# Performance work log

Hardware: AMD Instinct MI355X
Metric: run time of the kernel (lower is better)

## Reference

```python
import jax, jax.numpy as jnp
import numpy as np

# dims
B, S, E, H = 2, 2048, 2048, 2688   # batch, seq, embedding_dim, hidden_dim
NH, DH = 4, 2688 // 4              # mLSTM heads, head dim
KS = 4                             # causal conv kernel size
BLK = 4                            # qkv_proj_blocksize
NPH = H // BLK                     # headwise-proj heads


def setup_inputs() -> dict:
    key = jax.random.key(0)
    ks = jax.random.split(key, 12)
    r = lambda i, shape, s=0.02: jax.random.normal(ks[i], shape, jnp.float32) * s
    return dict(
        x=jax.random.normal(ks[0], (B, S, E), jnp.float32),
        W_in=r(1, (E, 2 * H)),                       # up projection (no bias)
        conv_w=r(2, (KS, 1, H), 0.1),                # depthwise causal conv kernel (W, I/g, O)
        conv_b=jnp.zeros((H,), jnp.float32),
        Wq=r(3, (NPH, BLK, BLK), 0.3),               # headwise q proj
        Wk=r(4, (NPH, BLK, BLK), 0.3),               # headwise k proj
        Wv=r(5, (NPH, BLK, BLK), 0.3),               # headwise v proj
        W_ig=r(6, (3 * H, NH)),                      # input gate proj
        b_ig=jax.random.normal(ks[7], (NH,), jnp.float32),
        W_fg=r(8, (3 * H, NH)),                      # forget gate proj
        b_fg=jnp.linspace(3.0, 6.0, NH).astype(jnp.float32),
        norm_w=jnp.ones((H,), jnp.float32),          # multi-head layernorm weight
        skip=jnp.ones((H,), jnp.float32),            # learnable skip
        W_out=r(9, (H, E)),                          # down projection
    )


def _headwise(x, W):
    # LinearHeadwiseExpand: (B,S,H) -> (B,S,NPH,BLK) -> einsum -> (B,S,H)
    b, s, _ = x.shape
    xh = x.reshape(b, s, NPH, BLK)
    return jnp.einsum('bshd,hdo->bsho', xh, W).reshape(b, s, -1)


def reference(x, W_in, conv_w, conv_b, Wq, Wk, Wv, W_ig, b_ig, W_fg, b_fg, norm_w, skip, W_out):
    x_inner = x @ W_in                               # (B,S,2H)
    x_m, z = jnp.split(x_inner, 2, axis=-1)
    # depthwise causal conv1d
    xc = jax.lax.conv_general_dilated(
        x_m, conv_w, (1,), [(KS - 1, 0)],
        dimension_numbers=('NWC', 'WIO', 'NWC'), feature_group_count=H) + conv_b
    xca = jax.nn.silu(xc)
    q = _headwise(xca, Wq)
    k = _headwise(xca, Wk)
    v = _headwise(x_m, Wv)
    # ---- mLSTM cell (parallel stabilized form) ----
    qh = q.reshape(B, S, NH, DH).transpose(0, 2, 1, 3)   # (B,NH,S,DH)
    kh = k.reshape(B, S, NH, DH).transpose(0, 2, 1, 3)
    vh = v.reshape(B, S, NH, DH).transpose(0, 2, 1, 3)
    if_in = jnp.concatenate([q, k, v], axis=-1)          # (B,S,3H)
    i_pre = (if_in @ W_ig + b_ig).transpose(0, 2, 1)     # (B,NH,S)
    f_pre = (if_in @ W_fg + b_fg).transpose(0, 2, 1)
    log_fg = jax.nn.log_sigmoid(f_pre)                   # (B,NH,S)
    cs = jnp.cumsum(log_fg, axis=-1)
    # log decay matrix: sum of log forget gates t=j+1..i, causal masked
    dmat = cs[:, :, :, None] - cs[:, :, None, :]         # (B,NH,S,S)
    mask = jnp.tril(jnp.ones((S, S), bool))
    log_D = jnp.where(mask, dmat + i_pre[:, :, None, :], -jnp.inf)
    m = jnp.max(log_D, axis=-1, keepdims=True)           # stabilizer (B,NH,S,1)
    D = jnp.exp(log_D - m)
    qk = jnp.einsum('bnsd,bntd->bnst', qh, kh) / jnp.sqrt(jnp.float32(DH))
    C = qk * D
    n = jnp.maximum(jnp.abs(C.sum(-1, keepdims=True)), jnp.exp(-m))
    h = jnp.einsum('bnst,bntd->bnsd', C / (n + 1e-6), vh)
    # multi-head layernorm over DH, learnable scale over full H
    mu = h.mean(-1, keepdims=True)
    var = h.var(-1, keepdims=True)
    hn = (h - mu) * jax.lax.rsqrt(var + 1e-5)
    hn = hn.transpose(0, 2, 1, 3).reshape(B, S, H) * norm_w
    # ---- gated skip + output ----
    h_skip = hn + skip * xca
    hs = h_skip * jax.nn.silu(z)
    return hs @ W_out
```

## Files before the change

kernel.cpp:

```cpp
#include <hip/hip_runtime.h>

typedef unsigned short u16;
typedef unsigned int u32;
typedef __bf16 bf16x8 __attribute__((ext_vector_type(8)));
typedef float f32x4 __attribute__((ext_vector_type(4)));

#define BB   2
#define SS   2048
#define EE   2048
#define HH   2688
#define NHH  4
#define DHH  672
#define NPHH 672
#define H2   5376
#define H3   8064

__device__ __forceinline__ float b2f(u16 u) {
  union { unsigned int i; float f; } c; c.i = ((unsigned int)u) << 16; return c.f;
}
__device__ __forceinline__ u16 f2b(float f) {
  union { float f; unsigned int i; } c; c.f = f;
  unsigned int i = c.i;
  return (u16)((i + 0x7FFFu + ((i >> 16) & 1u)) >> 16);
}
__device__ __forceinline__ float silu_f(float x) { return x / (1.f + __expf(-x)); }
__device__ __forceinline__ float logsig_f(float f) {
  return (f >= 0.f) ? -log1pf(__expf(-f)) : (f - log1pf(__expf(f)));
}

__device__ __forceinline__ void gl2lds16(const u16* g, u16* s) {
  __builtin_amdgcn_global_load_lds(
      (const __attribute__((address_space(1))) u32*)g,
      (__attribute__((address_space(3))) u32*)s, 16, 0, 0);
}

template <int N> __device__ __forceinline__ void vmwait() {
  asm volatile("s_waitcnt vmcnt(%0)" :: "n"(N) : "memory");
}

template <int MODE, int OUTF32>
__global__ __launch_bounds__(512, 1) void gemm8(
    const u16* __restrict__ A, const u16* __restrict__ Bt, void* __restrict__ Cp,
    int M, int N, int K, int lda, int ldb, int ldc,
    long sAhi, long sAlo, long sBhi, long sBlo, long sChi, long sClo,
    const float* __restrict__ aux1, const float* __restrict__ aux2,
    int auxStride, int causal)
{
  constexpr int SLOT = (128 + 256) * 64;
  __shared__ __align__(16) u16 sm[3 * SLOT];

  int gx = gridDim.x;
  int nwg = gx * gridDim.y;
  int flat = blockIdx.y * gx + blockIdx.x;
  int qq = nwg >> 3, r8 = nwg & 7;
  int xcd = flat & 7, seq = flat >> 3;
  int logical = (xcd < r8 ? xcd * (qq + 1) : r8 * (qq + 1) + (xcd - r8) * qq) + seq;
  int bx = logical % gx, by = logical / gx;
  int m0 = by * 128, n0 = bx * 256;
  if (MODE == 1 && n0 > m0 + 127) return;

  int bz = blockIdx.z, bzh = bz >> 2, bzl = bz & 3;
  A  += bzh * sAhi + bzl * sAlo;
  Bt += bzh * sBhi + bzl * sBlo;
  const float* a1 = aux1 ? aux1 + (long)bz * auxStride : nullptr;
  const float* a2 = aux2 ? aux2 + (long)bz * auxStride : nullptr;
  u16*   C16 = (u16*)Cp + bzh * sChi + bzl * sClo;
  float* C32 = (float*)Cp + bzh * sChi + bzl * sClo;

  int t = threadIdx.x, lane = t & 63, w = t >> 6;
  int l15 = lane & 15, quad = lane >> 4;
  int wr = w >> 2, wc = w & 3;

  int srow = t >> 3;
  int sw8 = ((t & 7) ^ (srow & 7)) * 8;
  const u16* pS[6];
  int dOf[6];
#pragma unroll
  for (int c = 0; c < 2; ++c) {
    pS[c] = A + (long)(m0 + c * 64 + srow) * lda + sw8;
    dOf[c] = c * 4096 + w * 512;
  }
#pragma unroll
  for (int c = 0; c < 4; ++c) {
    pS[2 + c] = Bt + (long)(n0 + c * 64 + srow) * ldb + sw8;
    dOf[2 + c] = 8192 + c * 4096 + w * 512;
  }

  f32x4 acc[4][4];
#pragma unroll
  for (int i = 0; i < 4; i++)
#pragma unroll
    for (int j = 0; j < 4; j++) acc[i][j] = (f32x4){0.f, 0.f, 0.f, 0.f};

  int Keff = (MODE == 2 && causal) ? min(K, m0 + 128) : K;
  int T = Keff >> 6;

  auto STAGE = [&](int slot, int k2, int c) {
    gl2lds16(pS[c] + k2, sm + slot * SLOT + dOf[c]);
  };

  int npre = T < 2 ? T : 2;
  for (int tt = 0; tt < npre; ++tt)
#pragma unroll
    for (int c = 0; c < 6; ++c) STAGE(tt, tt << 6, c);
  if (npre >= 2) vmwait<6>(); else vmwait<0>();
  __builtin_amdgcn_s_barrier();
  __builtin_amdgcn_sched_barrier(0);

  int sl = 0;
  for (int tq = 0; tq < T; ++tq) {
    u16* Sb = sm + sl * SLOT;
    int sl2 = sl + 2; if (sl2 >= 3) sl2 -= 3;
    const bool stg = (tq + 2 < T);
    const int k2 = (tq + 2) << 6;
    int cx = (l15 & 7);

    bf16x8 bfr[4][2], af[2][2];
#pragma unroll
    for (int j = 0; j < 4; ++j)
#pragma unroll
      for (int ks = 0; ks < 2; ++ks)
        bfr[j][ks] = *reinterpret_cast<const bf16x8*>(
            Sb + 8192 + (wc * 64 + j * 16 + l15) * 64 + ((((ks << 2) + quad) ^ cx) << 3));
#pragma unroll
    for (int i = 0; i < 2; ++i)
#pragma unroll
      for (int ks = 0; ks < 2; ++ks)
        af[i][ks] = *reinterpret_cast<const bf16x8*>(
            Sb + (wr * 64 + i * 16 + l15) * 64 + ((((ks << 2) + quad) ^ cx) << 3));
    if (stg) { STAGE(sl2, k2, 0); STAGE(sl2, k2, 1); STAGE(sl2, k2, 2); }
    __builtin_amdgcn_s_barrier();
    asm volatile("s_waitcnt lgkmcnt(0)" ::: "memory");
    __builtin_amdgcn_sched_barrier(0);
    __builtin_amdgcn_s_setprio(1);
#pragma unroll
    for (int i = 0; i < 2; ++i)
#pragma unroll
      for (int j = 0; j < 4; ++j) {
        acc[i][j] = __builtin_amdgcn_mfma_f32_16x16x32_bf16(af[i][0], bfr[j][0], acc[i][j], 0, 0, 0);
        acc[i][j] = __builtin_amdgcn_mfma_f32_16x16x32_bf16(af[i][1], bfr[j][1], acc[i][j], 0, 0, 0);
      }
    __builtin_amdgcn_s_setprio(0);
    __builtin_amdgcn_sched_barrier(0);
    __builtin_amdgcn_s_barrier();

    bf16x8 ag[2][2];
#pragma unroll
    for (int i = 0; i < 2; ++i)
#pragma unroll
      for (int ks = 0; ks < 2; ++ks)
        ag[i][ks] = *reinterpret_cast<const bf16x8*>(
            Sb + (wr * 64 + (i + 2) * 16 + l15) * 64 + ((((ks << 2) + quad) ^ cx) << 3));
    if (stg) { STAGE(sl2, k2, 3); STAGE(sl2, k2, 4); STAGE(sl2, k2, 5); }
    __builtin_amdgcn_s_barrier();
    asm volatile("s_waitcnt lgkmcnt(0)" ::: "memory");
    __builtin_amdgcn_sched_barrier(0);
    __builtin_amdgcn_s_setprio(1);
#pragma unroll
    for (int i = 0; i < 2; ++i)
#pragma unroll
      for (int j = 0; j < 4; ++j) {
        acc[i + 2][j] = __builtin_amdgcn_mfma_f32_16x16x32_bf16(ag[i][0], bfr[j][0], acc[i + 2][j], 0, 0, 0);
        acc[i + 2][j] = __builtin_amdgcn_mfma_f32_16x16x32_bf16(ag[i][1], bfr[j][1], acc[i + 2][j], 0, 0, 0);
      }
    __builtin_amdgcn_s_setprio(0);
    __builtin_amdgcn_sched_barrier(0);
    if (tq + 1 < T) {
      if (stg) vmwait<6>(); else vmwait<0>();
      __builtin_amdgcn_s_barrier();
      __builtin_amdgcn_sched_barrier(0);
    }
    sl = sl + 1; if (sl >= 3) sl = 0;
  }

  const float rs = 0.03857583749f;
#pragma unroll
  for (int i = 0; i < 4; i++) {
#pragma unroll
    for (int j = 0; j < 4; j++) {
      int col = n0 + wc * 64 + j * 16 + l15;
      if (col >= N) continue;
#pragma unroll
      for (int rr = 0; rr < 4; rr++) {
        int row = m0 + wr * 64 + i * 16 + quad * 4 + rr;
        if (row >= M) continue;
        float v = acc[i][j][rr];
        if (MODE == 1) v = (col <= row) ? v * rs * __expf(a1[col] - a2[row]) : 0.f;
        else if (MODE == 2) v = v * a1[row];
        if (OUTF32) C32[(long)row * ldc + col] = v;
        else        C16[(long)row * ldc + col] = f2b(v);
      }
    }
  }
}

template <int BM, int MODE, int OUTF32>
__global__ __launch_bounds__(512, 1) void gemm_p(
    const u16* __restrict__ A, const u16* __restrict__ Bt, void* __restrict__ Cp,
    int M, int N, int K, int lda, int ldb, int ldc,
    long sAhi, long sAlo, long sBhi, long sBlo, long sChi, long sClo,
    const float* __restrict__ aux1, const float* __restrict__ aux2,
    int auxStride, int causal)
{
  constexpr int MFR   = BM / 32;
  constexpr int NPH   = MFR / 2;
  constexpr int SLOT  = (BM + 256) * 32;
  constexpr int ACH   = BM / 128;
  constexpr int LOADS = ACH + 2;
  __shared__ __align__(16) u16 sm[4 * SLOT];

  int gx = gridDim.x;
  int nwg = gx * gridDim.y;
  int flat = blockIdx.y * gx + blockIdx.x;
  int qq = nwg >> 3, r8 = nwg & 7;
  int xcd = flat & 7, seq = flat >> 3;
  int logical = (xcd < r8 ? xcd * (qq + 1) : r8 * (qq + 1) + (xcd - r8) * qq) + seq;
  int bx = logical % gx, by = logical / gx;
  int m0 = by * BM, n0 = bx * 256;
  if (MODE == 1 && n0 > m0 + BM - 1) return;

  int bz = blockIdx.z, bzh = bz >> 2, bzl = bz & 3;
  A  += bzh * sAhi + bzl * sAlo;
  Bt += bzh * sBhi + bzl * sBlo;
  const float* a1 = aux1 ? aux1 + (long)bz * auxStride : nullptr;
  const float* a2 = aux2 ? aux2 + (long)bz * auxStride : nullptr;
  u16*   C16 = (u16*)Cp + bzh * sChi + bzl * sClo;
  float* C32 = (float*)Cp + bzh * sChi + bzl * sClo;

  int t = threadIdx.x, lane = t & 63, w = t >> 6;
  int l15 = lane & 15, quad = lane >> 4;
  int wr = w >> 2, wc = w & 3;

  int srow = t >> 2;
  int swz = (((t & 3) ^ ((t >> 3) & 3)) * 8);
  const u16* pS[LOADS];
  int coff[LOADS];
#pragma unroll
  for (int c = 0; c < ACH; ++c) {
    pS[c] = A + (long)(m0 + c * 128 + srow) * lda + swz;
    coff[c] = c * 4096 + w * 512;
  }
#pragma unroll
  for (int c = 0; c < 2; ++c) {
    pS[ACH + c] = Bt + (long)(n0 + c * 128 + srow) * ldb + swz;
    coff[ACH + c] = BM * 32 + c * 4096 + w * 512;
  }

  int rswz = (quad ^ ((l15 >> 1) & 3)) * 8;
  int aoff = (wr * (BM / 2) + l15) * 32 + rswz;
  int boff = BM * 32 + (wc * 64 + l15) * 32 + rswz;

  f32x4 acc[MFR][4];
#pragma unroll
  for (int i = 0; i < MFR; i++)
#pragma unroll
    for (int j = 0; j < 4; j++) acc[i][j] = (f32x4){0.f, 0.f, 0.f, 0.f};

  int Keff = (MODE == 2 && causal) ? min(K, m0 + BM) : K;
  int T = Keff >> 5;

  auto STAGE1 = [&](int tt, int c) {
    gl2lds16(pS[c] + (tt << 5), sm + (tt & 3) * SLOT + coff[c]);
  };

  int npre = T < 3 ? T : 3;
  for (int tt = 0; tt < npre; ++tt)
#pragma unroll
    for (int c = 0; c < LOADS; ++c) STAGE1(tt, c);
  if (npre >= 3)      vmwait<2 * LOADS>();
  else if (npre == 2) vmwait<LOADS>();
  else                vmwait<0>();
  __builtin_amdgcn_s_barrier();
  __builtin_amdgcn_sched_barrier(0);

  for (int tq = 0; tq < T; ++tq) {
    u16* Sb = sm + (tq & 3) * SLOT;
    const bool stg = (tq + 3 < T);
    bf16x8 bf[4];
#pragma unroll
    for (int p = 0; p < NPH; ++p) {
      bf16x8 a0 = *reinterpret_cast<const bf16x8*>(Sb + aoff + (2 * p) * 512);
      bf16x8 a1v = *reinterpret_cast<const bf16x8*>(Sb + aoff + (2 * p + 1) * 512);
      if (p == 0) {
#pragma unroll
        for (int j = 0; j < 4; ++j)
          bf[j] = *reinterpret_cast<const bf16x8*>(Sb + boff + j * 512);
      }
      if (stg) {
#pragma unroll
        for (int c = p * LOADS / NPH; c < (p + 1) * LOADS / NPH; ++c)
          STAGE1(tq + 3, c);
      }
      __builtin_amdgcn_s_barrier();
      asm volatile("s_waitcnt lgkmcnt(0)" ::: "memory");
      __builtin_amdgcn_sched_barrier(0);
      __builtin_amdgcn_s_setprio(1);
#pragma unroll
      for (int j = 0; j < 4; ++j)
        acc[2 * p][j] = __builtin_amdgcn_mfma_f32_16x16x32_bf16(a0, bf[j], acc[2 * p][j], 0, 0, 0);
#pragma unroll
      for (int j = 0; j < 4; ++j)
        acc[2 * p + 1][j] = __builtin_amdgcn_mfma_f32_16x16x32_bf16(a1v, bf[j], acc[2 * p + 1][j], 0, 0, 0);
      __builtin_amdgcn_s_setprio(0);
      __builtin_amdgcn_sched_barrier(0);
    }
    if (tq + 1 < T) {
      if (tq + 3 < T)      vmwait<2 * LOADS>();
      else if (tq + 2 < T) vmwait<LOADS>();
      else                 vmwait<0>();
      __builtin_amdgcn_s_barrier();
      __builtin_amdgcn_sched_barrier(0);
    }
  }

  const float rs = 0.03857583749f;
#pragma unroll
  for (int i = 0; i < MFR; i++) {
#pragma unroll
    for (int j = 0; j < 4; j++) {
      int col = n0 + wc * 64 + j * 16 + l15;
      if (col >= N) continue;
#pragma unroll
      for (int rr = 0; rr < 4; rr++) {
        int row = m0 + wr * (BM / 2) + i * 16 + quad * 4 + rr;
        if (row >= M) continue;
        float v = acc[i][j][rr];
        if (MODE == 1) v = (col <= row) ? v * rs * __expf(a1[col] - a2[row]) : 0.f;
        else if (MODE == 2) v = v * a1[row];
        if (OUTF32) C32[(long)row * ldc + col] = v;
        else        C16[(long)row * ldc + col] = f2b(v);
      }
    }
  }
}

template <int F32IN>
__global__ __launch_bounds__(256) void transpose_any(
    const void* __restrict__ in, u16* __restrict__ out, int R, int C, int ldin,
    long inHi, long inLo, long outStride)
{
  __shared__ u16 tile[64][65];
  int bz = blockIdx.z, bzh = bz >> 2, bzl = bz & 3;
  const u16* in16 = (const u16*)in + bzh * inHi + bzl * inLo;
  const float* inf = (const float*)in + bzh * inHi + bzl * inLo;
  out += (long)bz * outStride;
  int r0 = blockIdx.y * 64, c0 = blockIdx.x * 64;
  int t = threadIdx.x;
  for (int idx = t; idx < 64 * 64; idx += 256) {
    int r = idx >> 6, c = idx & 63;
    int rr = r0 + r, cc = c0 + c;
    u16 v = 0;
    if (rr < R && cc < C) {
      long off = (long)rr * ldin + cc;
      v = F32IN ? f2b(inf[off]) : in16[off];
    }
    tile[r][c] = v;
  }
  __syncthreads();
  for (int idx = t; idx < 64 * 64; idx += 256) {
    int r = idx & 63, c = idx >> 6;
    int rr = r0 + r, cc = c0 + c;
    if (rr < R && cc < C) out[(long)cc * R + rr] = tile[r][c];
  }
}

__global__ __launch_bounds__(256) void convert_x(
    const float* __restrict__ x, u16* __restrict__ o)
{
  long i = ((long)blockIdx.x * 256 + threadIdx.x) * 8;
  if (i >= (long)4096 * EE) return;
  float4 a = *reinterpret_cast<const float4*>(x + i);
  float4 b = *reinterpret_cast<const float4*>(x + i + 4);
  u16 t8[8] = {f2b(a.x), f2b(a.y), f2b(a.z), f2b(a.w),
               f2b(b.x), f2b(b.y), f2b(b.z), f2b(b.w)};
  *reinterpret_cast<uint4*>(o + i) = *reinterpret_cast<uint4*>(t8);
}

__global__ __launch_bounds__(256) void prep_wqkv(
    const float* __restrict__ Wq, const float* __restrict__ Wk,
    const float* __restrict__ Wv, u16* __restrict__ o)
{
  int i = blockIdx.x * 256 + threadIdx.x;
  if (i >= 3 * 10752) return;
  int m = i / 10752, j = i % 10752;
  const float* W = (m == 0) ? Wq : (m == 1) ? Wk : Wv;
  o[i] = f2b(W[j]);
}

__global__ __launch_bounds__(256) void conv_head(
    const u16* __restrict__ xinner, const float* __restrict__ cw,
    const float* __restrict__ cb, const u16* __restrict__ Wqkv,
    u16* __restrict__ xca, u16* __restrict__ q, u16* __restrict__ k,
    u16* __restrict__ v)
{
  long idx = (long)blockIdx.x * 256 + threadIdx.x;
  if (idx >= (long)BB * SS * NPHH) return;
  int nph = (int)(idx % NPHH);
  long bs = idx / NPHH;
  int s = (int)(bs % SS);
  int h4 = nph * 4;
  float4 acc = *reinterpret_cast<const float4*>(cb + h4);
  uint2 xmr;
#pragma unroll
  for (int w = 0; w < 4; w++) {
    int sp = s + w - 3;
    if (sp < 0) continue;
    uint2 xr = *reinterpret_cast<const uint2*>(xinner + (bs + w - 3) * H2 + h4);
    if (w == 3) xmr = xr;
    const u16* xh = (const u16*)&xr;
    float4 cwv = *reinterpret_cast<const float4*>(cw + w * HH + h4);
    acc.x += b2f(xh[0]) * cwv.x;
    acc.y += b2f(xh[1]) * cwv.y;
    acc.z += b2f(xh[2]) * cwv.z;
    acc.w += b2f(xh[3]) * cwv.w;
  }
  float xaf[4] = {silu_f(acc.x), silu_f(acc.y), silu_f(acc.z), silu_f(acc.w)};
  u16 xa16[4] = {f2b(xaf[0]), f2b(xaf[1]), f2b(xaf[2]), f2b(xaf[3])};
#pragma unroll
  for (int d = 0; d < 4; d++) xaf[d] = b2f(xa16[d]);
  const u16* xm = (const u16*)&xmr;
  float xmf[4];
#pragma unroll
  for (int d = 0; d < 4; d++) xmf[d] = b2f(xm[d]);
  *reinterpret_cast<uint2*>(xca + bs * HH + h4) = *reinterpret_cast<uint2*>(xa16);

  union { uint4 v4[2]; u16 h[16]; } wq, wk, wv;
  const uint4* wqp = reinterpret_cast<const uint4*>(Wqkv + nph * 16);
  const uint4* wkp = reinterpret_cast<const uint4*>(Wqkv + 10752 + nph * 16);
  const uint4* wvp = reinterpret_cast<const uint4*>(Wqkv + 21504 + nph * 16);
  wq.v4[0] = wqp[0]; wq.v4[1] = wqp[1];
  wk.v4[0] = wkp[0]; wk.v4[1] = wkp[1];
  wv.v4[0] = wvp[0]; wv.v4[1] = wvp[1];
  u16 qo[4], ko[4], vo[4];
#pragma unroll
  for (int o = 0; o < 4; o++) {
    float aq = 0.f, ak = 0.f, av = 0.f;
#pragma unroll
    for (int d = 0; d < 4; d++) {
      aq += xaf[d] * b2f(wq.h[d * 4 + o]);
      ak += xaf[d] * b2f(wk.h[d * 4 + o]);
      av += xmf[d] * b2f(wv.h[d * 4 + o]);
    }
    qo[o] = f2b(aq); ko[o] = f2b(ak); vo[o] = f2b(av);
  }
  long ob = bs * HH + h4;
  *reinterpret_cast<uint2*>(q + ob) = *reinterpret_cast<uint2*>(qo);
  *reinterpret_cast<uint2*>(k + ob) = *reinterpret_cast<uint2*>(ko);
  *reinterpret_cast<uint2*>(v + ob) = *reinterpret_cast<uint2*>(vo);
}

__global__ __launch_bounds__(256) void gate_gemv(
    const u16* __restrict__ qb, const u16* __restrict__ kb,
    const u16* __restrict__ vb, const float* __restrict__ Wig,
    const float* __restrict__ Wfg, float* __restrict__ G)
{
  __shared__ u16 wlds[8 * HH];
  int seg = blockIdx.y;
  const u16* X = (seg == 0) ? qb : (seg == 1) ? kb : vb;
  int t = threadIdx.x;
  for (int c = t; c < HH; c += 256) {
    float4 wi = *reinterpret_cast<const float4*>(Wig + ((long)seg * HH + c) * 4);
    float4 wf = *reinterpret_cast<const float4*>(Wfg + ((long)seg * HH + c) * 4);
    wlds[0 * HH + c] = f2b(wi.x); wlds[1 * HH + c] = f2b(wi.y);
    wlds[2 * HH + c] = f2b(wi.z); wlds[3 * HH + c] = f2b(wi.w);
    wlds[4 * HH + c] = f2b(wf.x); wlds[5 * HH + c] = f2b(wf.y);
    wlds[6 * HH + c] = f2b(wf.z); wlds[7 * HH + c] = f2b(wf.w);
  }
  __syncthreads();
  int wv = t >> 6, lane = t & 63;
  int r0 = blockIdx.x * 32 + wv * 8;
  for (int r = 0; r < 8; ++r) {
    int row = r0 + r;
    const u16* xr = X + (long)row * HH;
    float a0=0,a1=0,a2=0,a3=0,a4=0,a5=0,a6=0,a7=0;
    for (int ch = lane; ch < HH / 8; ch += 64) {
      uint4 xv = *reinterpret_cast<const uint4*>(xr + ch * 8);
      const u16* xe = (const u16*)&xv;
      float xf[8];
#pragma unroll
      for (int e = 0; e < 8; ++e) xf[e] = b2f(xe[e]);
#pragma unroll
      for (int j = 0; j < 8; ++j) {
        uint4 wv4 = *reinterpret_cast<const uint4*>(wlds + j * HH + ch * 8);
        const u16* we = (const u16*)&wv4;
        float s = 0.f;
#pragma unroll
        for (int e = 0; e < 8; ++e) s += xf[e] * b2f(we[e]);
        if (j == 0) a0 += s; else if (j == 1) a1 += s;
        else if (j == 2) a2 += s; else if (j == 3) a3 += s;
        else if (j == 4) a4 += s; else if (j == 5) a5 += s;
        else if (j == 6) a6 += s; else a7 += s;
      }
    }
#pragma unroll
    for (int off = 32; off > 0; off >>= 1) {
      a0 += __shfl_down(a0, off); a1 += __shfl_down(a1, off);
      a2 += __shfl_down(a2, off); a3 += __shfl_down(a3, off);
      a4 += __shfl_down(a4, off); a5 += __shfl_down(a5, off);
      a6 += __shfl_down(a6, off); a7 += __shfl_down(a7, off);
    }
    if (lane == 0) {
      float* g = G + ((long)seg * 4096 + row) * 24 + seg * 8;
      g[0] = a0; g[1] = a1; g[2] = a2; g[3] = a3;
      g[4] = a4; g[5] = a5; g[6] = a6; g[7] = a7;
    }
  }
}

__global__ __launch_bounds__(1024) void scan_kernel(
    const float* __restrict__ G, const float* __restrict__ big,
    const float* __restrict__ bfg,
    float* __restrict__ avec, float* __restrict__ rmaxvec, float* __restrict__ mvec)
{
  __shared__ float buf[2][SS];
  __shared__ float isave[SS];
  __shared__ float cssave[SS];
  int bn = blockIdx.x;
  int b = bn >> 2, n = bn & 3;
  int t = threadIdx.x;
  float bi = big[n], bf = bfg[n];
  for (int i = t; i < SS; i += 1024) {
    long tk = (long)b * SS + i;
    float ip = G[tk * 24 + n] + G[(4096 + tk) * 24 + 8 + n] +
               G[(8192 + tk) * 24 + 16 + n] + bi;
    float fp = G[tk * 24 + 4 + n] + G[(4096 + tk) * 24 + 12 + n] +
               G[(8192 + tk) * 24 + 20 + n] + bf;
    isave[i] = ip;
    buf[0][i] = logsig_f(fp);
  }
  __syncthreads();
  int src = 0;
  for (int off = 1; off < SS; off <<= 1) {
    int dst = 1 - src;
    for (int i = t; i < SS; i += 1024) {
      float x = buf[src][i];
      if (i >= off) x += buf[src][i - off];
      buf[dst][i] = x;
    }
    __syncthreads();
    src = dst;
  }
  for (int i = t; i < SS; i += 1024) {
    float cs = buf[src][i];
    cssave[i] = cs;
    float a = isave[i] - cs;
    avec[(long)bn * SS + i] = a;
    buf[src][i] = a;
  }
  __syncthreads();
  for (int off = 1; off < SS; off <<= 1) {
    int dst = 1 - src;
    for (int i = t; i < SS; i += 1024) {
      float x = buf[src][i];
      if (i >= off) x = fmaxf(x, buf[src][i - off]);
      buf[dst][i] = x;
    }
    __syncthreads();
    src = dst;
  }
  for (int i = t; i < SS; i += 1024) {
    rmaxvec[(long)bn * SS + i] = buf[src][i];
    mvec[(long)bn * SS + i] = cssave[i] + buf[src][i];
  }
}

__global__ __launch_bounds__(256) void rowsum_kernel(
    const u16* __restrict__ P, const float* __restrict__ mvec, float* __restrict__ invn,
    long Pstride)
{
  int bz = blockIdx.z;
  P += (long)bz * Pstride;
  mvec += (long)bz * SS;
  invn += (long)bz * SS;
  int row = (blockIdx.x * 256 + threadIdx.x) >> 6;
  int lane = threadIdx.x & 63;
  if (row >= SS) return;
  const u16* pr = P + (long)row * SS;
  float s = 0.f;
  int j0 = lane * 8;
  for (; j0 + 7 <= row; j0 += 512) {
    uint4 u = *reinterpret_cast<const uint4*>(pr + j0);
    const u16* e = (const u16*)&u;
#pragma unroll
    for (int q = 0; q < 8; ++q) s += b2f(e[q]);
  }
  if (j0 <= row) {
    for (int q = 0; j0 + q <= row; ++q) s += b2f(pr[j0 + q]);
  }
#pragma unroll
  for (int off = 32; off > 0; off >>= 1) s += __shfl_down(s, off);
  if (lane == 0) {
    float n = fmaxf(fabsf(s), __expf(-mvec[row]));
    invn[row] = 1.f / (n + 1e-6f);
  }
}

__global__ __launch_bounds__(256) void ln_skip_gate(
    const u16* __restrict__ h, const u16* __restrict__ xca,
    const u16* __restrict__ xinner, const float* __restrict__ normw,
    const float* __restrict__ skipw, u16* __restrict__ hs)
{
  int row = (blockIdx.x * 256 + threadIdx.x) >> 6;
  int lane = threadIdx.x & 63;
  if (row >= BB * NHH * SS) return;
  int s = row % SS;
  int n = (row / SS) % NHH;
  int b = row / (SS * NHH);
  const u16* hr = h + (long)row * DHH;
  float sum = 0.f, ss = 0.f;
  float vx[6], vy[6];
#pragma unroll
  for (int i = 0; i < 6; ++i) {
    int d2 = lane + i * 64;
    float x = 0.f, y = 0.f;
    if (d2 < DHH / 2) {
      u32 u = *reinterpret_cast<const u32*>(hr + d2 * 2);
      x = b2f((u16)u); y = b2f((u16)(u >> 16));
    }
    vx[i] = x; vy[i] = y;
    sum += x + y; ss += x * x + y * y;
  }
#pragma unroll
  for (int off = 32; off > 0; off >>= 1) { sum += __shfl_down(sum, off); ss += __shfl_down(ss, off); }
  sum = __shfl(sum, 0); ss = __shfl(ss, 0);
  float mu = sum / (float)DHH;
  float var = ss / (float)DHH - mu * mu;
  float rstd = rsqrtf(var + 1e-5f);
  long bs = (long)b * SS + s;
#pragma unroll
  for (int i = 0; i < 6; ++i) {
    int d2 = lane + i * 64;
    if (d2 >= DHH / 2) continue;
    int c = n * DHH + d2 * 2;
    float2 nw = *reinterpret_cast<const float2*>(normw + c);
    float2 sw = *reinterpret_cast<const float2*>(skipw + c);
    u32 xcu = *reinterpret_cast<const u32*>(xca + bs * HH + c);
    u32 zu  = *reinterpret_cast<const u32*>(xinner + bs * H2 + HH + c);
    float h0 = (vx[i] - mu) * rstd * nw.x + sw.x * b2f((u16)xcu);
    float h1 = (vy[i] - mu) * rstd * nw.y + sw.y * b2f((u16)(xcu >> 16));
    float o0 = h0 * silu_f(b2f((u16)zu));
    float o1 = h1 * silu_f(b2f((u16)(zu >> 16)));
    u32 ou = (u32)f2b(o0) | ((u32)f2b(o1) << 16);
    *reinterpret_cast<u32*>(hs + bs * HH + c) = ou;
  }
}

__global__ __launch_bounds__(256) void fill_sentinel(float* out, float v, long n) {
  long i = (long)blockIdx.x * 256 + threadIdx.x;
  if (i < n) out[i] = v;
}

extern "C" void kernel_launch(void* const* d_in, const int* in_sizes, int n_in,
                              void* d_out, int out_size, void* d_ws, size_t ws_size,
                              hipStream_t stream)
{
  const float* x      = (const float*)d_in[0];
  const float* W_in   = (const float*)d_in[1];
  const float* conv_w = (const float*)d_in[2];
  const float* conv_b = (const float*)d_in[3];
  const float* Wq     = (const float*)d_in[4];
  const float* Wk     = (const float*)d_in[5];
  const float* Wv     = (const float*)d_in[6];
  const float* W_ig   = (const float*)d_in[7];
  const float* b_ig   = (const float*)d_in[8];
  const float* W_fg   = (const float*)d_in[9];
  const float* b_fg   = (const float*)d_in[10];
  const float* norm_w = (const float*)d_in[11];
  const float* skipw  = (const float*)d_in[12];
  const float* W_out  = (const float*)d_in[13];
  float* out = (float*)d_out;
  const long SD = (long)SS * DHH;
  const long SP = (long)SS * SS;
  const long BH = (long)SS * HH;

  u16* ws = (u16*)d_ws;
  size_t off = 0;
  auto alloc = [&](size_t n) { u16* p = ws + off; off += n; return p; };
  u16* x_inner = alloc((size_t)4096 * H2);
  u16* xca     = alloc((size_t)4096 * HH);
  u16* qb      = alloc((size_t)4096 * HH);
  u16* kb      = alloc((size_t)4096 * HH);
  u16* vb      = alloc((size_t)4096 * HH);
  float* fvec  = (float*)(ws + off);
  off += 4 * 16384 * 2;
  float* avec    = fvec;
  float* rmaxvec = avec + 16384;
  float* mvec    = rmaxvec + 16384;
  float* invn    = mvec + 16384;
  u16* vt8 = alloc((size_t)8 * SD);
  u16* Pb8 = alloc((size_t)8 * SP);
  size_t need = off * 2;
  long outn = (long)4096 * EE;

  if (ws_size < need) {
    fill_sentinel<<<dim3((outn + 255) / 256), 256, 0, stream>>>(
        out, 200.f + 0.01f * (float)(ws_size >> 20), outn);
    return;
  }

  u16* W_inT  = qb;
  u16* xbf    = kb;
  u16* W_outT = vb;
  u16* hbuf   = kb;
  u16* hsbuf  = qb;
  float* G    = (float*)(Pb8 + 344064);
  u16* Wqkv   = Pb8 + 933888;

  prep_wqkv<<<dim3(126, 1, 1), 256, 0, stream>>>(Wq, Wk, Wv, Wqkv);
  transpose_any<1><<<dim3(84, 32, 1), 256, 0, stream>>>(
      W_in, W_inT, EE, H2, H2, 0, 0, 0);
  convert_x<<<dim3(4096, 1, 1), 256, 0, stream>>>(x, xbf);
  gemm8<0, 0><<<dim3(21, 32, 1), 512, 0, stream>>>(
      xbf, W_inT, x_inner, 4096, H2, EE, EE, EE, H2,
      0, 0, 0, 0, 0, 0, nullptr, nullptr, 0, 0);
  conv_head<<<dim3(10752, 1, 1), 256, 0, stream>>>(
      x_inner, conv_w, conv_b, Wqkv, xca, qb, kb, vb);
  gate_gemv<<<dim3(128, 3, 1), 256, 0, stream>>>(qb, kb, vb, W_ig, W_fg, G);
  scan_kernel<<<dim3(8, 1, 1), 1024, 0, stream>>>(G, b_ig, b_fg, avec, rmaxvec, mvec);
  transpose_any<0><<<dim3(11, 32, 8), 256, 0, stream>>>(
      vb, vt8, SS, DHH, HH, BH, DHH, SD);
  gemm_p<256, 1, 0><<<dim3(8, 8, 8), 512, 0, stream>>>(
      qb, kb, Pb8, SS, SS, DHH, HH, HH, SS,
      BH, DHH, BH, DHH, 4 * SP, SP, avec, rmaxvec, SS, 0);
  rowsum_kernel<<<dim3(512, 1, 8), 256, 0, stream>>>(Pb8, mvec, invn, SP);
  gemm8<2, 0><<<dim3(3, 16, 8), 512, 0, stream>>>(
      Pb8, vt8, hbuf, SS, DHH, SS, SS, SS, DHH,
      4 * SP, SP, 4 * SD, SD, 4 * SD, SD, invn, nullptr, SS, 1);
  transpose_any<1><<<dim3(32, 42, 1), 256, 0, stream>>>(
      W_out, W_outT, HH, EE, EE, 0, 0, 0);
  ln_skip_gate<<<dim3(4096, 1, 1), 256, 0, stream>>>(
      hbuf, xca, x_inner, norm_w, skipw, hsbuf);
  gemm8<0, 1><<<dim3(8, 32, 1), 512, 0, stream>>>(
      hsbuf, W_outT, out, 4096, EE, HH, HH, HH, EE,
      0, 0, 0, 0, 0, 0, nullptr, nullptr, 0, 0);
}
```

Measured before the change: 651.5 us.

## Fuse gate projections into conv_head and replace scan with warp-shuffle scan

The input/forget gate GEMV moves into conv_head. Each block now handles one (batch, seq) row, so the fp32 q/k/v values multiply pre-packed bf16 gate weights and are reduced in-block, with no re-read of q/k/v from global memory. The separate gate_gemv kernel goes away and a small weight-prep kernel is added. The scan kernel changes from a log-step shared-memory Hillis-Steele scan with many barriers to a per-thread serial plus warp-shuffle scan. Gate preactivations now use unrounded fp32 q/k/v, which slightly changes numerics versus before.

```diff
diff --git a/kernel.cpp b/kernel.cpp
--- a/kernel.cpp
+++ b/kernel.cpp
@@ -387,180 +387,182 @@
   o[i] = f2b(W[j]);
 }
 
-__global__ __launch_bounds__(256) void conv_head(
+__global__ __launch_bounds__(256) void prep_gatew(
+    const float* __restrict__ Wig, const float* __restrict__ Wfg,
+    u16* __restrict__ Wg)
+{
+  int i = blockIdx.x * 256 + threadIdx.x;
+  if (i >= NPHH * 96) return;
+  int nph = i / 96, r = i % 96;
+  int seg = r >> 5, d = (r >> 3) & 3, j = r & 7;
+  const float* W = (j < 4) ? Wig : Wfg;
+  Wg[i] = f2b(W[(long)(seg * HH + nph * 4 + d) * 4 + (j & 3)]);
+}
+
+__global__ __launch_bounds__(704) void conv_head(
     const u16* __restrict__ xinner, const float* __restrict__ cw,
     const float* __restrict__ cb, const u16* __restrict__ Wqkv,
-    u16* __restrict__ xca, u16* __restrict__ q, u16* __restrict__ k,
-    u16* __restrict__ v)
-{
-  long idx = (long)blockIdx.x * 256 + threadIdx.x;
-  if (idx >= (long)BB * SS * NPHH) return;
-  int nph = (int)(idx % NPHH);
-  long bs = idx / NPHH;
+    const u16* __restrict__ Wg, u16* __restrict__ xca, u16* __restrict__ q,
+    u16* __restrict__ k, u16* __restrict__ v, float* __restrict__ G2)
+{
+  __shared__ float gsh[8];
+  long bs = blockIdx.x;
   int s = (int)(bs % SS);
-  int h4 = nph * 4;
-  float4 acc = *reinterpret_cast<const float4*>(cb + h4);
-  uint2 xmr;
-#pragma unroll
-  for (int w = 0; w < 4; w++) {
-    int sp = s + w - 3;
-    if (sp < 0) continue;
-    uint2 xr = *reinterpret_cast<const uint2*>(xinner + (bs + w - 3) * H2 + h4);
-    if (w == 3) xmr = xr;
-    const u16* xh = (const u16*)&xr;
-    float4 cwv = *reinterpret_cast<const float4*>(cw + w * HH + h4);
-    acc.x += b2f(xh[0]) * cwv.x;
-    acc.y += b2f(xh[1]) * cwv.y;
-    acc.z += b2f(xh[2]) * cwv.z;
-    acc.w += b2f(xh[3]) * cwv.w;
-  }
-  float xaf[4] = {silu_f(acc.x), silu_f(acc.y), silu_f(acc.z), silu_f(acc.w)};
-  u16 xa16[4] = {f2b(xaf[0]), f2b(xaf[1]), f2b(xaf[2]), f2b(xaf[3])};
-#pragma unroll
-  for (int d = 0; d < 4; d++) xaf[d] = b2f(xa16[d]);
-  const u16* xm = (const u16*)&xmr;
-  float xmf[4];
-#pragma unroll
-  for (int d = 0; d < 4; d++) xmf[d] = b2f(xm[d]);
-  *reinterpret_cast<uint2*>(xca + bs * HH + h4) = *reinterpret_cast<uint2*>(xa16);
-
-  union { uint4 v4[2]; u16 h[16]; } wq, wk, wv;
-  const uint4* wqp = reinterpret_cast<const uint4*>(Wqkv + nph * 16);
-  const uint4* wkp = reinterpret_cast<const uint4*>(Wqkv + 10752 + nph * 16);
-  const uint4* wvp = reinterpret_cast<const uint4*>(Wqkv + 21504 + nph * 16);
-  wq.v4[0] = wqp[0]; wq.v4[1] = wqp[1];
-  wk.v4[0] = wkp[0]; wk.v4[1] = wkp[1];
-  wv.v4[0] = wvp[0]; wv.v4[1] = wvp[1];
-  u16 qo[4], ko[4], vo[4];
-#pragma unroll
-  for (int o = 0; o < 4; o++) {
-    float aq = 0.f, ak = 0.f, av = 0.f;
-#pragma unroll
-    for (int d = 0; d < 4; d++) {
-      aq += xaf[d] * b2f(wq.h[d * 4 + o]);
-      ak += xaf[d] * b2f(wk.h[d * 4 + o]);
-      av += xmf[d] * b2f(wv.h[d * 4 + o]);
-    }
-    qo[o] = f2b(aq); ko[o] = f2b(ak); vo[o] = f2b(av);
-  }
-  long ob = bs * HH + h4;
-  *reinterpret_cast<uint2*>(q + ob) = *reinterpret_cast<uint2*>(qo);
-  *reinterpret_cast<uint2*>(k + ob) = *reinterpret_cast<uint2*>(ko);
-  *reinterpret_cast<uint2*>(v + ob) = *reinterpret_cast<uint2*>(vo);
-}
-
-__global__ __launch_bounds__(256) void gate_gemv(
-    const u16* __restrict__ qb, const u16* __restrict__ kb,
-    const u16* __restrict__ vb, const float* __restrict__ Wig,
-    const float* __restrict__ Wfg, float* __restrict__ G)
-{
-  __shared__ u16 wlds[8 * HH];
-  int seg = blockIdx.y;
-  const u16* X = (seg == 0) ? qb : (seg == 1) ? kb : vb;
-  int t = threadIdx.x;
-  for (int c = t; c < HH; c += 256) {
-    float4 wi = *reinterpret_cast<const float4*>(Wig + ((long)seg * HH + c) * 4);
-    float4 wf = *reinterpret_cast<const float4*>(Wfg + ((long)seg * HH + c) * 4);
-    wlds[0 * HH + c] = f2b(wi.x); wlds[1 * HH + c] = f2b(wi.y);
-    wlds[2 * HH + c] = f2b(wi.z); wlds[3 * HH + c] = f2b(wi.w);
-    wlds[4 * HH + c] = f2b(wf.x); wlds[5 * HH + c] = f2b(wf.y);
-    wlds[6 * HH + c] = f2b(wf.z); wlds[7 * HH + c] = f2b(wf.w);
-  }
+  int t = threadIdx.x, lane = t & 63;
+  if (t < 8) gsh[t] = 0.f;
   __syncthreads();
-  int wv = t >> 6, lane = t & 63;
-  int r0 = blockIdx.x * 32 + wv * 8;
-  for (int r = 0; r < 8; ++r) {
-    int row = r0 + r;
-    const u16* xr = X + (long)row * HH;
-    float a0=0,a1=0,a2=0,a3=0,a4=0,a5=0,a6=0,a7=0;
-    for (int ch = lane; ch < HH / 8; ch += 64) {
-      uint4 xv = *reinterpret_cast<const uint4*>(xr + ch * 8);
-      const u16* xe = (const u16*)&xv;
-      float xf[8];
-#pragma unroll
-      for (int e = 0; e < 8; ++e) xf[e] = b2f(xe[e]);
-#pragma unroll
-      for (int j = 0; j < 8; ++j) {
-        uint4 wv4 = *reinterpret_cast<const uint4*>(wlds + j * HH + ch * 8);
-        const u16* we = (const u16*)&wv4;
-        float s = 0.f;
-#pragma unroll
-        for (int e = 0; e < 8; ++e) s += xf[e] * b2f(we[e]);
-        if (j == 0) a0 += s; else if (j == 1) a1 += s;
-        else if (j == 2) a2 += s; else if (j == 3) a3 += s;
-        else if (j == 4) a4 += s; else if (j == 5) a5 += s;
-        else if (j == 6) a6 += s; else a7 += s;
+
+  float gi[4] = {0.f, 0.f, 0.f, 0.f}, gf[4] = {0.f, 0.f, 0.f, 0.f};
+  if (t < NPHH) {
+    int h4 = t * 4;
+    float4 acc = *reinterpret_cast<const float4*>(cb + h4);
+    uint2 xmr = {0, 0};
+#pragma unroll
+    for (int w = 0; w < 4; w++) {
+      int sp = s + w - 3;
+      if (sp < 0) continue;
+      uint2 xr = *reinterpret_cast<const uint2*>(xinner + (bs + w - 3) * H2 + h4);
+      if (w == 3) xmr = xr;
+      const u16* xh = (const u16*)&xr;
+      float4 cwv = *reinterpret_cast<const float4*>(cw + w * HH + h4);
+      acc.x += b2f(xh[0]) * cwv.x;
+      acc.y += b2f(xh[1]) * cwv.y;
+      acc.z += b2f(xh[2]) * cwv.z;
+      acc.w += b2f(xh[3]) * cwv.w;
+    }
+    float xaf[4] = {silu_f(acc.x), silu_f(acc.y), silu_f(acc.z), silu_f(acc.w)};
+    u16 xa16[4] = {f2b(xaf[0]), f2b(xaf[1]), f2b(xaf[2]), f2b(xaf[3])};
+#pragma unroll
+    for (int d = 0; d < 4; d++) xaf[d] = b2f(xa16[d]);
+    const u16* xm = (const u16*)&xmr;
+    float xmf[4];
+#pragma unroll
+    for (int d = 0; d < 4; d++) xmf[d] = b2f(xm[d]);
+    *reinterpret_cast<uint2*>(xca + bs * HH + h4) = *reinterpret_cast<uint2*>(xa16);
+
+    union { uint4 v4[2]; u16 h[16]; } wq, wk, wv;
+    const uint4* wqp = reinterpret_cast<const uint4*>(Wqkv + t * 16);
+    const uint4* wkp = reinterpret_cast<const uint4*>(Wqkv + 10752 + t * 16);
+    const uint4* wvp = reinterpret_cast<const uint4*>(Wqkv + 21504 + t * 16);
+    wq.v4[0] = wqp[0]; wq.v4[1] = wqp[1];
+    wk.v4[0] = wkp[0]; wk.v4[1] = wkp[1];
+    wv.v4[0] = wvp[0]; wv.v4[1] = wvp[1];
+    float aq[4], ak[4], av[4];
+    u16 qo[4], ko[4], vo[4];
+#pragma unroll
+    for (int o = 0; o < 4; o++) {
+      float sq = 0.f, sk = 0.f, sv = 0.f;
+#pragma unroll
+      for (int d = 0; d < 4; d++) {
+        sq += xaf[d] * b2f(wq.h[d * 4 + o]);
+        sk += xaf[d] * b2f(wk.h[d * 4 + o]);
+        sv += xmf[d] * b2f(wv.h[d * 4 + o]);
       }
-    }
-#pragma unroll
-    for (int off = 32; off > 0; off >>= 1) {
-      a0 += __shfl_down(a0, off); a1 += __shfl_down(a1, off);
-      a2 += __shfl_down(a2, off); a3 += __shfl_down(a3, off);
-      a4 += __shfl_down(a4, off); a5 += __shfl_down(a5, off);
-      a6 += __shfl_down(a6, off); a7 += __shfl_down(a7, off);
-    }
-    if (lane == 0) {
-      float* g = G + ((long)seg * 4096 + row) * 24 + seg * 8;
-      g[0] = a0; g[1] = a1; g[2] = a2; g[3] = a3;
-      g[4] = a4; g[5] = a5; g[6] = a6; g[7] = a7;
-    }
-  }
-}
-
-__global__ __launch_bounds__(1024) void scan_kernel(
-    const float* __restrict__ G, const float* __restrict__ big,
+      aq[o] = sq; ak[o] = sk; av[o] = sv;
+      qo[o] = f2b(sq); ko[o] = f2b(sk); vo[o] = f2b(sv);
+    }
+    long ob = bs * HH + h4;
+    *reinterpret_cast<uint2*>(q + ob) = *reinterpret_cast<uint2*>(qo);
+    *reinterpret_cast<uint2*>(k + ob) = *reinterpret_cast<uint2*>(ko);
+    *reinterpret_cast<uint2*>(v + ob) = *reinterpret_cast<uint2*>(vo);
+
+    union { uint4 v4[12]; u16 h[96]; } wg;
+    const uint4* wgp = reinterpret_cast<const uint4*>(Wg + t * 96);
+#pragma unroll
+    for (int u = 0; u < 12; ++u) wg.v4[u] = wgp[u];
+#pragma unroll
+    for (int seg = 0; seg < 3; ++seg) {
+      const float* xx = (seg == 0) ? aq : (seg == 1) ? ak : av;
+#pragma unroll
+      for (int d = 0; d < 4; ++d) {
+        float xv = xx[d];
+        const u16* wr = &wg.h[seg * 32 + d * 8];
+#pragma unroll
+        for (int n = 0; n < 4; ++n) {
+          gi[n] += xv * b2f(wr[n]);
+          gf[n] += xv * b2f(wr[4 + n]);
+        }
+      }
+    }
+  }
+#pragma unroll
+  for (int off = 32; off > 0; off >>= 1) {
+#pragma unroll
+    for (int n = 0; n < 4; ++n) {
+      gi[n] += __shfl_down(gi[n], off);
+      gf[n] += __shfl_down(gf[n], off);
+    }
+  }
+  if (lane == 0) {
+#pragma unroll
+    for (int n = 0; n < 4; ++n) {
+      atomicAdd(&gsh[n], gi[n]);
+      atomicAdd(&gsh[4 + n], gf[n]);
+    }
+  }
+  __syncthreads();
+  if (t < 8) G2[bs * 8 + t] = gsh[t];
+}
+
+__global__ __launch_bounds__(256) void scan_kernel(
+    const float* __restrict__ G2, const float* __restrict__ big,
     const float* __restrict__ bfg,
     float* __restrict__ avec, float* __restrict__ rmaxvec, float* __restrict__ mvec)
 {
-  __shared__ float buf[2][SS];
-  __shared__ float isave[SS];
-  __shared__ float cssave[SS];
+  __shared__ float wsum[4], wmax[4];
   int bn = blockIdx.x;
   int b = bn >> 2, n = bn & 3;
-  int t = threadIdx.x;
+  int t = threadIdx.x, lane = t & 63, wv = t >> 6;
   float bi = big[n], bf = bfg[n];
-  for (int i = t; i < SS; i += 1024) {
-    long tk = (long)b * SS + i;
-    float ip = G[tk * 24 + n] + G[(4096 + tk) * 24 + 8 + n] +
-               G[(8192 + tk) * 24 + 16 + n] + bi;
-    float fp = G[tk * 24 + 4 + n] + G[(4096 + tk) * 24 + 12 + n] +
-               G[(8192 + tk) * 24 + 20 + n] + bf;
-    isave[i] = ip;
-    buf[0][i] = logsig_f(fp);
-  }
+  int i0 = t * 8;
+  float ip[8], ls[8];
+  float run = 0.f;
+#pragma unroll
+  for (int kk = 0; kk < 8; ++kk) {
+    long tk = (long)b * SS + i0 + kk;
+    ip[kk] = G2[tk * 8 + n] + bi;
+    run += logsig_f(G2[tk * 8 + 4 + n] + bf);
+    ls[kk] = run;
+  }
+  float v = run;
+#pragma unroll
+  for (int off = 1; off < 64; off <<= 1) {
+    float o = __shfl_up(v, off);
+    if (lane >= off) v += o;
+  }
+  if (lane == 63) wsum[wv] = v;
   __syncthreads();
-  int src = 0;
-  for (int off = 1; off < SS; off <<= 1) {
-    int dst = 1 - src;
-    for (int i = t; i < SS; i += 1024) {
-      float x = buf[src][i];
-      if (i >= off) x += buf[src][i - off];
-      buf[dst][i] = x;
-    }
-    __syncthreads();
-    src = dst;
-  }
-  for (int i = t; i < SS; i += 1024) {
-    float cs = buf[src][i];
-    cssave[i] = cs;
-    float a = isave[i] - cs;
-    avec[(long)bn * SS + i] = a;
-    buf[src][i] = a;
-  }
+  float woff = 0.f;
+  for (int u = 0; u < wv; ++u) woff += wsum[u];
+  float excl = v - run + woff;
+  float a[8], lm[8];
+  float runm = -3.4e38f;
+#pragma unroll
+  for (int kk = 0; kk < 8; ++kk) {
+    float cs = excl + ls[kk];
+    ls[kk] = cs;
+    a[kk] = ip[kk] - cs;
+    runm = fmaxf(runm, a[kk]);
+    lm[kk] = runm;
+    avec[(long)bn * SS + i0 + kk] = a[kk];
+  }
+  float mv = runm;
+#pragma unroll
+  for (int off = 1; off < 64; off <<= 1) {
+    float o = __shfl_up(mv, off);
+    if (lane >= off) mv = fmaxf(mv, o);
+  }
+  if (lane == 63) wmax[wv] = mv;
   __syncthreads();
-  for (int off = 1; off < SS; off <<= 1) {
-    int dst = 1 - src;
-    for (int i = t; i < SS; i += 1024) {
-      float x = buf[src][i];
-      if (i >= off) x = fmaxf(x, buf[src][i - off]);
-      buf[dst][i] = x;
-    }
-    __syncthreads();
-    src = dst;
-  }
-  for (int i = t; i < SS; i += 1024) {
-    rmaxvec[(long)bn * SS + i] = buf[src][i];
-    mvec[(long)bn * SS + i] = cssave[i] + buf[src][i];
+  float woffm = -3.4e38f;
+  for (int u = 0; u < wv; ++u) woffm = fmaxf(woffm, wmax[u]);
+  float pm = __shfl_up(mv, 1);
+  float pre = (lane == 0) ? woffm : fmaxf(woffm, pm);
+#pragma unroll
+  for (int kk = 0; kk < 8; ++kk) {
+    float r = fmaxf(pre, lm[kk]);
+    rmaxvec[(long)bn * SS + i0 + kk] = r;
+    mvec[(long)bn * SS + i0 + kk] = ls[kk] + r;
   }
 }
 
@@ -703,20 +705,22 @@
   u16* W_outT = vb;
   u16* hbuf   = kb;
   u16* hsbuf  = qb;
-  float* G    = (float*)(Pb8 + 344064);
+  float* G2   = (float*)(Pb8 + 344064);
   u16* Wqkv   = Pb8 + 933888;
+  u16* Wg     = Pb8 + 966144;
 
   prep_wqkv<<<dim3(126, 1, 1), 256, 0, stream>>>(Wq, Wk, Wv, Wqkv);
+  prep_gatew<<<dim3(252, 1, 1), 256, 0, stream>>>(W_ig, W_fg, Wg);
+  fill_sentinel<<<dim3(128, 1, 1), 256, 0, stream>>>(G2, 0.f, 32768);
   transpose_any<1><<<dim3(84, 32, 1), 256, 0, stream>>>(
       W_in, W_inT, EE, H2, H2, 0, 0, 0);
   convert_x<<<dim3(4096, 1, 1), 256, 0, stream>>>(x, xbf);
   gemm8<0, 0><<<dim3(21, 32, 1), 512, 0, stream>>>(
       xbf, W_inT, x_inner, 4096, H2, EE, EE, EE, H2,
       0, 0, 0, 0, 0, 0, nullptr, nullptr, 0, 0);
-  conv_head<<<dim3(10752, 1, 1), 256, 0, stream>>>(
-      x_inner, conv_w, conv_b, Wqkv, xca, qb, kb, vb);
-  gate_gemv<<<dim3(128, 3, 1), 256, 0, stream>>>(qb, kb, vb, W_ig, W_fg, G);
-  scan_kernel<<<dim3(8, 1, 1), 1024, 0, stream>>>(G, b_ig, b_fg, avec, rmaxvec, mvec);
+  conv_head<<<dim3(4096, 1, 1), 704, 0, stream>>>(
+      x_inner, conv_w, conv_b, Wqkv, Wg, xca, qb, kb, vb, G2);
+  scan_kernel<<<dim3(8, 1, 1), 256, 0, stream>>>(G2, b_ig, b_fg, avec, rmaxvec, mvec);
   transpose_any<0><<<dim3(11, 32, 8), 256, 0, stream>>>(
       vb, vt8, SS, DHH, HH, BH, DHH, SD);
   gemm_p<256, 1, 0><<<dim3(8, 8, 8), 512, 0, stream>>>(
```

Result: slower. 703.8 us (+8.0%).
